# Optimization experiments

Hardware: AMD Instinct MI355X
Metric: run time of the kernel (lower is better)

## Reference

```python
import jax, jax.numpy as jnp
import numpy as np

EPS = 1e-5  # torch BatchNorm2d default eps


def _bn(x, gamma, beta, mean, var):
    # inference-mode BatchNorm2d: x [B,C,H,W], params [C]
    inv = gamma / jnp.sqrt(var + EPS)
    return x * inv[None, :, None, None] + (beta - mean * inv)[None, :, None, None]


def _conv1x1(x, W, b=None):
    # 1x1 conv == per-pixel matmul. x [B,C,H,W], W [O,C]
    y = jnp.einsum('bchw,oc->bohw', x, W)
    if b is not None:
        y = y + b[None, :, None, None]
    return y


def _resize_bilinear_ac(x, H, W):
    # bilinear upsample with align_corners=True, separable gather + lerp
    h, w = x.shape[2], x.shape[3]
    ys = jnp.linspace(0.0, h - 1.0, H)
    xs = jnp.linspace(0.0, w - 1.0, W)
    y0 = jnp.floor(ys).astype(jnp.int32); y1 = jnp.minimum(y0 + 1, h - 1)
    x0 = jnp.floor(xs).astype(jnp.int32); x1 = jnp.minimum(x0 + 1, w - 1)
    wy = (ys - y0).astype(x.dtype)
    wx = (xs - x0).astype(x.dtype)
    rows = x[:, :, y0, :] * (1 - wy)[None, None, :, None] + x[:, :, y1, :] * wy[None, None, :, None]
    out = rows[:, :, :, x0] * (1 - wx) + rows[:, :, :, x1] * wx
    return out


def setup_inputs() -> dict:
    key = jax.random.key(0)
    ks = jax.random.split(key, 11)
    B, C, H, W = 8, 512, 96, 96
    Kd, Vd, Od = 256, 256, 512
    s = lambda k, shape: jax.random.normal(k, shape, jnp.float32)
    return dict(
        x=s(ks[0], (B, C, H, W)),
        Wk=s(ks[1], (Kd, C)) * 0.05,                      # shared query/key 1x1 conv
        k_gamma=jnp.ones((Kd,), jnp.float32), k_beta=jnp.zeros((Kd,), jnp.float32),
        k_mean=s(ks[2], (Kd,)) * 0.1, k_var=jnp.abs(s(ks[3], (Kd,))) + 0.5,
        Wv=s(ks[4], (Vd, C)) * 0.05, bv=s(ks[5], (Vd,)) * 0.05,   # value 1x1 conv
        Ww=s(ks[6], (Od, Vd)) * 0.05, bw=s(ks[7], (Od,)) * 0.05,  # 'weights' 1x1 conv (random instead of zero-init so output is nontrivial)
        Wr=s(ks[8], (Od, Od)) * 0.05,                             # refine 1x1 conv (in_dim==out_dim)
        r_gamma=jnp.ones((Od,), jnp.float32), r_beta=jnp.zeros((Od,), jnp.float32),
        r_mean=s(ks[9], (Od,)) * 0.1, r_var=jnp.abs(s(ks[10], (Od,))) + 0.5,
    )


def reference(x, Wk, k_gamma, k_beta, k_mean, k_var, Wv, bv, Ww, bw, Wr, r_gamma, r_beta, r_mean, r_var):
    B, C, H, W = x.shape
    scale = 2
    key_dim = Wk.shape[0]
    # MaxPool2d(scale, scale)
    xp = jax.lax.reduce_window(x, -jnp.inf, jax.lax.max,
                               (1, 1, scale, scale), (1, 1, scale, scale), 'VALID')
    h, w = xp.shape[2], xp.shape[3]
    N = h * w
    # query and key share the same conv+BN+ReLU (func_query = func_key)
    qk = jax.nn.relu(_bn(_conv1x1(xp, Wk), k_gamma, k_beta, k_mean, k_var)).reshape(B, key_dim, N)
    value = _conv1x1(xp, Wv, bv).reshape(B, -1, N)  # [B,Vd,N]
    # sim_map[b,n,m] = <query_n, key_m>, scaled then softmax over m
    sim = jnp.einsum('bkn,bkm->bnm', qk, qk) * (key_dim ** -0.5)
    attn = jax.nn.softmax(sim, axis=-1)
    ctx = jnp.einsum('bnm,bvm->bvn', attn, value).reshape(B, -1, h, w)  # [B,Vd,h,w]
    ctx = _conv1x1(ctx, Ww, bw)                      # -> [B,out_dim,h,w]
    ctx = _resize_bilinear_ac(ctx, H, W)             # align_corners=True bilinear
    out = jax.nn.relu(_bn(_conv1x1(ctx, Wr), r_gamma, r_beta, r_mean, r_var))
    return out
```

## Files before the change

### kernel.cpp

```cpp
#include <hip/hip_runtime.h>
#include <math.h>

typedef __attribute__((ext_vector_type(8))) short bf16x8;
typedef __attribute__((ext_vector_type(4))) float f32x4;

namespace {

constexpr int B_ = 8, C_ = 512, H_ = 96, W_ = 96;
constexpr int HP = 48, WP = 48, N_ = HP * WP;
constexpr int KD = 256, VD = 256, OD = 512;
constexpr int NSPLIT = 4;
constexpr float EPSV = 1e-5f;
constexpr float SCH = 0.30028060f;

constexpr size_t BOFF_XPT = 0;
constexpr size_t BOFF_QKT = BOFF_XPT + (size_t)B_ * N_ * C_ * 2;
constexpr size_t BOFF_VAL = BOFF_QKT + (size_t)B_ * N_ * KD * 2;
constexpr size_t BOFF_CTX = BOFF_VAL + (size_t)B_ * VD * N_ * 2;
constexpr size_t BOFF_W2  = BOFF_CTX + (size_t)B_ * N_ * VD * 2;
constexpr size_t BOFF_WF  = BOFF_W2  + (size_t)512 * 512 * 2;
constexpr size_t BOFF_BF  = BOFF_WF  + (size_t)OD * VD * 2;
constexpr size_t BOFF_PRT = BOFF_BF  + (size_t)OD * 4;
constexpr size_t BOFF_PM  = BOFF_PRT + (size_t)NSPLIT * B_ * N_ * VD * 2;
constexpr size_t BOFF_PL  = BOFF_PM  + (size_t)NSPLIT * B_ * N_ * 4;

}

__device__ __forceinline__ ushort f2bf(float f) {
    union { float f; unsigned u; } x; x.f = f;
    unsigned r = x.u + 0x7FFFu + ((x.u >> 16) & 1u);
    return (ushort)(r >> 16);
}

__device__ __forceinline__ float bf2f(ushort u) {
    union { unsigned u; float f; } x; x.u = ((unsigned)u) << 16;
    return x.f;
}

__device__ __forceinline__ void gload_lds16(const void* g, void* l) {
    __builtin_amdgcn_global_load_lds(
        (const __attribute__((address_space(1))) unsigned int*)g,
        (__attribute__((address_space(3))) unsigned int*)l, 16, 0, 0);
}

__global__ __launch_bounds__(192) void pool_t_kernel(const float* __restrict__ x,
                                                     ushort* __restrict__ xpT) {
    __shared__ float ps[64][49];
    const int gid = blockIdx.x;
    const int ct = gid & 7;
    const int tmp = gid >> 3;
    const int oh = tmp % 48;
    const int b  = tmp / 48;
    const int t = threadIdx.x;
    const int ow = t % 48, ci = t / 48;

    const int c0 = ct * 64;
#pragma unroll
    for (int pass = 0; pass < 16; ++pass) {
        const int c = pass * 4 + ci;
        const float* px = x + (((size_t)b * C_ + c0 + c) * H_ + 2 * oh) * W_ + 2 * ow;
        float2 a = *reinterpret_cast<const float2*>(px);
        float2 d = *reinterpret_cast<const float2*>(px + W_);
        ps[c][ow] = fmaxf(fmaxf(a.x, a.y), fmaxf(d.x, d.y));
    }
    __syncthreads();
    const int cc2 = (t & 31) * 2;
    const int nr0 = t >> 5;
#pragma unroll
    for (int pass = 0; pass < 8; ++pass) {
        const int nr = pass * 6 + nr0;
        ushort2 p2;
        p2.x = f2bf(ps[cc2][nr]);
        p2.y = f2bf(ps[cc2 + 1][nr]);
        *reinterpret_cast<ushort2*>(&xpT[((size_t)b * N_ + oh * 48 + nr) * C_ + c0 + cc2]) = p2;
    }
}

__global__ __launch_bounds__(256) void prep_kernel(const float* __restrict__ Wk,
                                                   const float* __restrict__ Wv,
                                                   const float* __restrict__ Wr,
                                                   const float* __restrict__ Ww,
                                                   const float* __restrict__ bw,
                                                   ushort* __restrict__ W2,
                                                   ushort* __restrict__ Wfb,
                                                   float* __restrict__ bfb) {
    const int blk = blockIdx.x;
    if (blk < 512) {
        const int m = blk;
        const float* src = (m < 256) ? (Wk + (size_t)m * 512) : (Wv + (size_t)(m - 256) * 512);
        const int k = threadIdx.x * 2;
        float2 v = *reinterpret_cast<const float2*>(src + k);
        ushort2 p; p.x = f2bf(v.x); p.y = f2bf(v.y);
        *reinterpret_cast<ushort2*>(&W2[(size_t)m * 512 + k]) = p;
    } else if (blk < 1024) {
        const int o = blk - 512;
        const int v = threadIdx.x;
        float s = 0.f;
        for (int c = 0; c < OD; ++c)
            s = fmaf(Wr[(size_t)o * OD + c], Ww[(size_t)c * VD + v], s);
        Wfb[(size_t)o * VD + v] = f2bf(s);
    } else {
        const int o = (blk - 1024) * 256 + threadIdx.x;
        float s = 0.f;
        for (int c = 0; c < OD; ++c) s = fmaf(Wr[(size_t)o * OD + c], bw[c], s);
        bfb[o] = s;
    }
}

__global__ __launch_bounds__(256) void qkv_mfma(
    const ushort* __restrict__ W2, const ushort* __restrict__ xpT,
    const float* __restrict__ kg, const float* __restrict__ kb,
    const float* __restrict__ km, const float* __restrict__ kv,
    const float* __restrict__ bv,
    ushort* __restrict__ qkT, ushort* __restrict__ val) {
    __shared__ ushort Al[2][4096];
    __shared__ ushort Bl[2][4096];

    const int id = blockIdx.x;
    const int b = id & 7;
    const int t = id >> 3;
    const int my = t & 7;
    const int nx = t >> 3;
    const int w = threadIdx.x >> 6, l = threadIdx.x & 63;
    const int lr = l & 15, lg = l >> 4;
    const int rbq = (lg * 8) ^ (((lr >> 1) & 3) << 3);

    const ushort* srcA = W2 + (size_t)(my * 64) * 512;
    const ushort* srcB = xpT + ((size_t)b * N_ + nx * 64) * 512;

    auto stage64 = [&](const ushort* src, int koff, char* lbase) {
#pragma unroll
        for (int j = 0; j < 2; ++j) {
            const int prow = j * 64 + w * 16 + (l >> 2);
            const int row = prow & 63;
            const int kc = prow >> 6;
            const int cb = ((l & 3) * 16) ^ (((row >> 1) & 3) << 4);
            const char* s = (const char*)(src + (size_t)row * 512 + koff) + kc * 64 + cb;
            gload_lds16(s, lbase + j * 4096 + w * 1024);
        }
    };

    stage64(srcA, 0, (char*)&Al[0][0]);
    stage64(srcB, 0, (char*)&Bl[0][0]);
    stage64(srcA, 64, (char*)&Al[1][0]);
    stage64(srcB, 64, (char*)&Bl[1][0]);

    f32x4 acc[4];
#pragma unroll
    for (int nt = 0; nt < 4; ++nt) acc[nt] = (f32x4){0.f, 0.f, 0.f, 0.f};

    for (int ks = 0; ks < 8; ++ks) {
        if (ks < 7) { asm volatile("s_waitcnt vmcnt(4)" ::: "memory"); }
        else        { asm volatile("s_waitcnt vmcnt(0)" ::: "memory"); }
        __builtin_amdgcn_s_barrier();
        __builtin_amdgcn_sched_barrier(0);
        const ushort* Ab = &Al[ks & 1][0];
        const ushort* Bb = &Bl[ks & 1][0];
        __builtin_amdgcn_s_setprio(1);
#pragma unroll
        for (int kc = 0; kc < 2; ++kc) {
            bf16x8 af = *reinterpret_cast<const bf16x8*>(Ab + kc * 2048 + (w * 16 + lr) * 32 + rbq);
#pragma unroll
            for (int nt = 0; nt < 4; ++nt) {
                bf16x8 bfr = *reinterpret_cast<const bf16x8*>(Bb + kc * 2048 + (nt * 16 + lr) * 32 + rbq);
                acc[nt] = __builtin_amdgcn_mfma_f32_16x16x32_bf16(af, bfr, acc[nt], 0, 0, 0);
            }
        }
        __builtin_amdgcn_s_setprio(0);
        __builtin_amdgcn_sched_barrier(0);
        __builtin_amdgcn_s_barrier();
        if (ks < 6) {
            stage64(srcA, (ks + 2) * 64, (char*)&Al[ks & 1][0]);
            stage64(srcB, (ks + 2) * 64, (char*)&Bl[ks & 1][0]);
        }
    }

    const int m0 = my * 64 + w * 16;
    if (m0 < 256) {
        float inv[4], add[4];
#pragma unroll
        for (int j = 0; j < 4; ++j) {
            int o = m0 + lg * 4 + j;
            inv[j] = kg[o] * rsqrtf(kv[o] + EPSV);
            add[j] = kb[o] - km[o] * inv[j];
        }
#pragma unroll
        for (int nt = 0; nt < 4; ++nt) {
            int n = nx * 64 + nt * 16 + lr;
            ushort4 q4;
            q4.x = f2bf(fmaxf(acc[nt][0] * inv[0] + add[0], 0.f) * SCH);
            q4.y = f2bf(fmaxf(acc[nt][1] * inv[1] + add[1], 0.f) * SCH);
            q4.z = f2bf(fmaxf(acc[nt][2] * inv[2] + add[2], 0.f) * SCH);
            q4.w = f2bf(fmaxf(acc[nt][3] * inv[3] + add[3], 0.f) * SCH);
            *reinterpret_cast<ushort4*>(&qkT[((size_t)b * N_ + n) * KD + m0 + lg * 4]) = q4;
        }
    } else {
#pragma unroll
        for (int j = 0; j < 4; ++j) {
            int vch = m0 - 256 + lg * 4 + j;
            float bb = bv[vch];
#pragma unroll
            for (int nt = 0; nt < 4; ++nt) {
                int n = nx * 64 + nt * 16 + lr;
                val[((size_t)b * VD + vch) * N_ + n] = f2bf(acc[nt][j] + bb);
            }
        }
    }
}

__global__ __launch_bounds__(256, 3) void attn_mfma(const ushort* __restrict__ qkT,
                                                    const ushort* __restrict__ val,
                                                    ushort* __restrict__ part,
                                                    float* __restrict__ pm,
                                                    float* __restrict__ pl) {
    __shared__ ushort Kl[2][8192];
    __shared__ ushort Vl[8192];
    __shared__ ushort Pl[4][512];

    const int id = blockIdx.x;
    const int b  = id & 7;
    const int rest = id >> 3;
    const int s  = rest & 3;
    const int qt = rest >> 2;
    const int q0 = qt * 64;
    const int t0 = s * 18;
    const int w  = threadIdx.x >> 6;
    const int l  = threadIdx.x & 63;
    const int lr = l & 15, lg = l >> 4;

    const ushort* Qb = qkT + (size_t)b * N_ * KD;
    const ushort* Vb = val + (size_t)b * VD * N_;

    const int rb = lr * 32 + ((lg * 8) ^ (((lr >> 1) & 3) << 3));

    bf16x8 qf[8];
    {
        const ushort* qrow = Qb + (size_t)(q0 + w * 16 + lr) * KD + lg * 8;
#pragma unroll
        for (int kc = 0; kc < 8; ++kc)
            qf[kc] = *reinterpret_cast<const bf16x8*>(qrow + kc * 32);
    }
    asm volatile("s_waitcnt vmcnt(0)" ::: "memory");

    auto stage_K = [&](int itx, int buf) {
#pragma unroll
        for (int j = 0; j < 4; ++j) {
            const int prow = j * 64 + w * 16 + (l >> 2);
            const int m = prow & 31;
            const int kc = prow >> 5;
            const int cb = ((l & 3) * 16) ^ (((m >> 1) & 3) << 4);
            const char* src = (const char*)Qb + (size_t)(itx * 32 + m) * (KD * 2) + kc * 64 + cb;
            gload_lds16(src, (char*)(&Kl[buf][0]) + j * 4096 + w * 1024);
        }
    };
    auto stage_V = [&](int itx) {
#pragma unroll
        for (int j = 0; j < 4; ++j) {
            const int r = j * 64 + w * 16 + (l >> 2);
            const int cb = ((l & 3) * 16) ^ (((r >> 1) & 3) << 4);
            const char* src = (const char*)Vb + (size_t)r * (N_ * 2) + itx * 64 + cb;
            gload_lds16(src, (char*)(&Vl[0]) + j * 4096 + w * 1024);
        }
    };

    stage_K(t0, 0);
    stage_V(t0);
    stage_K(t0 + 1, 1);

    f32x4 O[16];
#pragma unroll
    for (int vt = 0; vt < 16; ++vt) O[vt] = (f32x4){0.f, 0.f, 0.f, 0.f};
    f32x4 Ol = (f32x4){0.f, 0.f, 0.f, 0.f};
    float mrun[4] = {-1e30f, -1e30f, -1e30f, -1e30f};
    bf16x8 ones;
#pragma unroll
    for (int i = 0; i < 8; ++i) ones[i] = (short)0x3F80;

    ushort* Pw = &Pl[w][0];

    for (int it = 0; it < 18; ++it) {
        const int cur = it & 1;
        if (it < 17) { asm volatile("s_waitcnt vmcnt(8)" ::: "memory"); }
        else         { asm volatile("s_waitcnt vmcnt(4)" ::: "memory"); }
        __builtin_amdgcn_s_barrier();
        __builtin_amdgcn_sched_barrier(0);

        const ushort* Kc = &Kl[cur][0];

        f32x4 S0 = (f32x4){0.f, 0.f, 0.f, 0.f};
        f32x4 S1 = (f32x4){0.f, 0.f, 0.f, 0.f};
        __builtin_amdgcn_s_setprio(1);
#pragma unroll
        for (int kc = 0; kc < 8; ++kc) {
            bf16x8 k0 = *reinterpret_cast<const bf16x8*>(Kc + kc * 1024 + rb);
            bf16x8 k1 = *reinterpret_cast<const bf16x8*>(Kc + kc * 1024 + 512 + rb);
            S0 = __builtin_amdgcn_mfma_f32_16x16x32_bf16(qf[kc], k0, S0, 0, 0, 0);
            S1 = __builtin_amdgcn_mfma_f32_16x16x32_bf16(qf[kc], k1, S1, 0, 0, 0);
        }
        __builtin_amdgcn_s_setprio(0);

        float lmax[4];
        bool ok = true;
#pragma unroll
        for (int r = 0; r < 4; ++r) {
            lmax[r] = fmaxf(S0[r], S1[r]);
            ok = ok && (lmax[r] <= mrun[r] + 11.5f);
        }
        if (!__all(ok)) {
            float corr[4];
#pragma unroll
            for (int r = 0; r < 4; ++r) {
                float m2 = lmax[r];
#pragma unroll
                for (int off = 1; off < 16; off <<= 1) m2 = fmaxf(m2, __shfl_xor(m2, off, 16));
                const float mn = fmaxf(mrun[r], m2);
                corr[r] = exp2f(mrun[r] - mn);
                mrun[r] = mn;
            }
#pragma unroll
            for (int vt = 0; vt < 16; ++vt) {
                f32x4 o = O[vt];
                o[0] *= corr[0]; o[1] *= corr[1]; o[2] *= corr[2]; o[3] *= corr[3];
                O[vt] = o;
            }
            Ol[0] *= corr[0]; Ol[1] *= corr[1]; Ol[2] *= corr[2]; Ol[3] *= corr[3];
        }
#pragma unroll
        for (int r = 0; r < 4; ++r) {
            const int row = lg * 4 + r;
            const int sw = ((row >> 1) & 3) << 3;
            Pw[row * 32 + (lr ^ sw)] = f2bf(exp2f(S0[r] - mrun[r]));
            Pw[row * 32 + ((16 + lr) ^ sw)] = f2bf(exp2f(S1[r] - mrun[r]));
        }

        if (it < 17) { asm volatile("s_waitcnt vmcnt(4)" ::: "memory"); }
        else         { asm volatile("s_waitcnt vmcnt(0)" ::: "memory"); }
        __builtin_amdgcn_s_barrier();
        __builtin_amdgcn_sched_barrier(0);

        bf16x8 pf = *reinterpret_cast<const bf16x8*>(Pw + rb);
        __builtin_amdgcn_s_setprio(1);
        Ol = __builtin_amdgcn_mfma_f32_16x16x32_bf16(pf, ones, Ol, 0, 0, 0);
#pragma unroll
        for (int vt = 0; vt < 16; ++vt) {
            bf16x8 vf = *reinterpret_cast<const bf16x8*>(Vl + vt * 512 + rb);
            O[vt] = __builtin_amdgcn_mfma_f32_16x16x32_bf16(pf, vf, O[vt], 0, 0, 0);
        }
        __builtin_amdgcn_s_setprio(0);

        __builtin_amdgcn_sched_barrier(0);
        __builtin_amdgcn_s_barrier();
        if (it < 17) stage_V(t0 + it + 1);
        if (it < 16) stage_K(t0 + it + 2, cur);
    }

    float il[4];
#pragma unroll
    for (int r = 0; r < 4; ++r) il[r] = 1.0f / Ol[r];
    ushort* Pp = part + (((size_t)s * B_ + b) * N_ + q0 + w * 16) * VD;
#pragma unroll
    for (int vt = 0; vt < 16; ++vt) {
#pragma unroll
        for (int j = 0; j < 4; ++j)
            Pp[(size_t)(lg * 4 + j) * VD + vt * 16 + lr] = f2bf(O[vt][j] * il[j]);
    }
    if (lr == 0) {
#pragma unroll
        for (int r = 0; r < 4; ++r) {
            const size_t idx = ((size_t)s * B_ + b) * N_ + q0 + w * 16 + lg * 4 + r;
            pm[idx] = mrun[r];
            pl[idx] = Ol[r];
        }
    }
}

__global__ __launch_bounds__(256) void merge_kernel(const ushort* __restrict__ part,
                                                    const float* __restrict__ pm,
                                                    const float* __restrict__ pl,
                                                    ushort* __restrict__ ctxT) {
    const int row = blockIdx.x * 8 + (threadIdx.x >> 5);
    const int lane = threadIdx.x & 31;
    const size_t RN = (size_t)B_ * N_;

    float m[NSPLIT], lv[NSPLIT];
#pragma unroll
    for (int si = 0; si < NSPLIT; ++si) {
        m[si]  = pm[si * RN + row];
        lv[si] = pl[si * RN + row];
    }
    float M = fmaxf(fmaxf(m[0], m[1]), fmaxf(m[2], m[3]));
    float wgt[NSPLIT], wsum = 0.f;
#pragma unroll
    for (int si = 0; si < NSPLIT; ++si) {
        wgt[si] = exp2f(m[si] - M) * lv[si];
        wsum += wgt[si];
    }
    const float inv = 1.0f / wsum;

    float acc[8] = {};
#pragma unroll
    for (int si = 0; si < NSPLIT; ++si) {
        bf16x8 p = *reinterpret_cast<const bf16x8*>(&part[(si * RN + row) * VD + lane * 8]);
        const float ws = wgt[si];
#pragma unroll
        for (int j = 0; j < 8; ++j) acc[j] = fmaf(ws, bf2f((ushort)p[j]), acc[j]);
    }
    ushort4 o0, o1;
    o0.x = f2bf(acc[0] * inv); o0.y = f2bf(acc[1] * inv);
    o0.z = f2bf(acc[2] * inv); o0.w = f2bf(acc[3] * inv);
    o1.x = f2bf(acc[4] * inv); o1.y = f2bf(acc[5] * inv);
    o1.z = f2bf(acc[6] * inv); o1.w = f2bf(acc[7] * inv);
    ushort* dst = ctxT + (size_t)row * VD + lane * 8;
    *reinterpret_cast<ushort4*>(dst) = o0;
    *reinterpret_cast<ushort4*>(dst + 4) = o1;
}

__global__ __launch_bounds__(256) void out_mfma(const ushort* __restrict__ Wfb,
                                                const float* __restrict__ bfuse,
                                                const float* __restrict__ rg,
                                                const float* __restrict__ rbta,
                                                const float* __restrict__ rm,
                                                const float* __restrict__ rv,
                                                const ushort* __restrict__ ctxT,
                                                ushort* __restrict__ Z) {
    __shared__ ushort Al[2][4096];
    __shared__ ushort Bl[2][4096];

    const int id = blockIdx.x;
    const int b = id & 7;
    const int t = id >> 3;
    const int my = t & 7;
    const int nx = t >> 3;
    const int w = threadIdx.x >> 6, l = threadIdx.x & 63;
    const int lr = l & 15, lg = l >> 4;
    const int rbq = (lg * 8) ^ (((lr >> 1) & 3) << 3);

    const ushort* srcA = Wfb + (size_t)(my * 64) * VD;
    const ushort* srcB = ctxT + ((size_t)b * N_ + nx * 64) * VD;

    auto stage64 = [&](const ushort* src, int koff, char* lbase) {
#pragma unroll
        for (int j = 0; j < 2; ++j) {
            const int prow = j * 64 + w * 16 + (l >> 2);
            const int row = prow & 63;
            const int kc = prow >> 6;
            const int cb = ((l & 3) * 16) ^ (((row >> 1) & 3) << 4);
            const char* s = (const char*)(src + (size_t)row * VD + koff) + kc * 64 + cb;
            gload_lds16(s, lbase + j * 4096 + w * 1024);
        }
    };

    stage64(srcA, 0, (char*)&Al[0][0]);
    stage64(srcB, 0, (char*)&Bl[0][0]);
    stage64(srcA, 64, (char*)&Al[1][0]);
    stage64(srcB, 64, (char*)&Bl[1][0]);

    f32x4 acc[4];
#pragma unroll
    for (int nt = 0; nt < 4; ++nt) acc[nt] = (f32x4){0.f, 0.f, 0.f, 0.f};

    for (int ks = 0; ks < 4; ++ks) {
        if (ks < 3) { asm volatile("s_waitcnt vmcnt(4)" ::: "memory"); }
        else        { asm volatile("s_waitcnt vmcnt(0)" ::: "memory"); }
        __builtin_amdgcn_s_barrier();
        __builtin_amdgcn_sched_barrier(0);
        const ushort* Ab = &Al[ks & 1][0];
        const ushort* Bb = &Bl[ks & 1][0];
        __builtin_amdgcn_s_setprio(1);
#pragma unroll
        for (int kc = 0; kc < 2; ++kc) {
            bf16x8 af = *reinterpret_cast<const bf16x8*>(Ab + kc * 2048 + (w * 16 + lr) * 32 + rbq);
#pragma unroll
            for (int nt = 0; nt < 4; ++nt) {
                bf16x8 bfr = *reinterpret_cast<const bf16x8*>(Bb + kc * 2048 + (nt * 16 + lr) * 32 + rbq);
                acc[nt] = __builtin_amdgcn_mfma_f32_16x16x32_bf16(af, bfr, acc[nt], 0, 0, 0);
            }
        }
        __builtin_amdgcn_s_setprio(0);
        __builtin_amdgcn_sched_barrier(0);
        __builtin_amdgcn_s_barrier();
        if (ks < 2) {
            stage64(srcA, (ks + 2) * 64, (char*)&Al[ks & 1][0]);
            stage64(srcB, (ks + 2) * 64, (char*)&Bl[ks & 1][0]);
        }
    }

    const int m0 = my * 64 + w * 16;
#pragma unroll
    for (int j = 0; j < 4; ++j) {
        const int o = m0 + lg * 4 + j;
        const float inv = rg[o] * rsqrtf(rv[o] + EPSV);
        const float add = rbta[o] - rm[o] * inv;
        const float bb = bfuse[o];
#pragma unroll
        for (int nt = 0; nt < 4; ++nt) {
            const int n = nx * 64 + nt * 16 + lr;
            Z[((size_t)b * OD + o) * N_ + n] = f2bf((acc[nt][j] + bb) * inv + add);
        }
    }
}

__global__ void upsample_kernel(const ushort* __restrict__ Z,
                                float* __restrict__ out) {
    const int total = B_ * OD * H_ * (W_ / 4);
    const float s = 47.0f / 95.0f;
    for (int idx = blockIdx.x * blockDim.x + threadIdx.x; idx < total;
         idx += gridDim.x * blockDim.x) {
        const int xq = idx % 24;
        const int t = idx / 24;
        const int y = t % H_;
        const int bo = t / H_;
        const float fy = y * s;
        const int y0 = (int)fy;
        const int y1 = min(y0 + 1, HP - 1);
        const float wy = fy - y0;
        const ushort* Zp = Z + (size_t)bo * N_;
        const ushort* r0 = Zp + y0 * WP;
        const ushort* r1 = Zp + y1 * WP;
        float4 o4;
        float* po = &o4.x;
#pragma unroll
        for (int j = 0; j < 4; ++j) {
            const int x = xq * 4 + j;
            const float fx = x * s;
            const int x0 = (int)fx;
            const int x1 = min(x0 + 1, WP - 1);
            const float wx = fx - x0;
            float v00 = bf2f(r0[x0]), v01 = bf2f(r0[x1]);
            float v10 = bf2f(r1[x0]), v11 = bf2f(r1[x1]);
            float a = v00 + (v01 - v00) * wx;
            float c = v10 + (v11 - v10) * wx;
            po[j] = fmaxf(a + (c - a) * wy, 0.f);
        }
        *reinterpret_cast<float4*>(out + (size_t)idx * 4) = o4;
    }
}

extern "C" void kernel_launch(void* const* d_in, const int* in_sizes, int n_in,
                              void* d_out, int out_size, void* d_ws, size_t ws_size,
                              hipStream_t stream) {
    const float* x  = (const float*)d_in[0];
    const float* Wk = (const float*)d_in[1];
    const float* kg = (const float*)d_in[2];
    const float* kb = (const float*)d_in[3];
    const float* km = (const float*)d_in[4];
    const float* kvv= (const float*)d_in[5];
    const float* Wv = (const float*)d_in[6];
    const float* bv = (const float*)d_in[7];
    const float* Ww = (const float*)d_in[8];
    const float* bw = (const float*)d_in[9];
    const float* Wr = (const float*)d_in[10];
    const float* rg = (const float*)d_in[11];
    const float* rb = (const float*)d_in[12];
    const float* rm = (const float*)d_in[13];
    const float* rv = (const float*)d_in[14];

    char* wsb = (char*)d_ws;
    ushort* xpT  = (ushort*)(wsb + BOFF_XPT);
    ushort* qkT  = (ushort*)(wsb + BOFF_QKT);
    ushort* valp = (ushort*)(wsb + BOFF_VAL);
    ushort* ctxT = (ushort*)(wsb + BOFF_CTX);
    ushort* W2   = (ushort*)(wsb + BOFF_W2);
    ushort* Wfb  = (ushort*)(wsb + BOFF_WF);
    float*  bfb  = (float*)(wsb + BOFF_BF);
    ushort* part = (ushort*)(wsb + BOFF_PRT);
    float*  pm   = (float*)(wsb + BOFF_PM);
    float*  pl   = (float*)(wsb + BOFF_PL);
    ushort* Z    = (ushort*)(wsb + BOFF_XPT);
    float*  out  = (float*)d_out;

    pool_t_kernel<<<8 * 48 * 8, 192, 0, stream>>>(x, xpT);
    prep_kernel<<<1026, 256, 0, stream>>>(Wk, Wv, Wr, Ww, bw, W2, Wfb, bfb);
    qkv_mfma<<<2304, 256, 0, stream>>>(W2, xpT, kg, kb, km, kvv, bv, qkT, valp);
    attn_mfma<<<1152, 256, 0, stream>>>(qkT, valp, part, pm, pl);
    merge_kernel<<<(B_ * N_) / 8, 256, 0, stream>>>(part, pm, pl, ctxT);
    out_mfma<<<2304, 256, 0, stream>>>(Wfb, bfb, rg, rb, rm, rv, ctxT, Z);
    upsample_kernel<<<4096, 256, 0, stream>>>(Z, out);
}
```

Before: 262.7 us.

## Split PV matmul across waves by value channels, sharing P tiles via LDS

```diff
diff --git a/kernel.cpp b/kernel.cpp
--- a/kernel.cpp
+++ b/kernel.cpp
@@ -213,16 +213,19 @@
                                                     ushort* __restrict__ part,
                                                     float* __restrict__ pm,
                                                     float* __restrict__ pl) {
-    __shared__ ushort Kl[2][8192];
-    __shared__ ushort Vl[8192];
-    __shared__ ushort Pl[4][512];
+    __shared__ __align__(16) ushort Kl[2][8192];
+    __shared__ __align__(16) ushort Vl[8192];
+    __shared__ __align__(16) ushort Pl[4][512];
+    __shared__ __align__(16) float corr_s[4][16];
+    __shared__ __align__(16) float il_s[4][16];
+    __shared__ __align__(16) int   flg[4];
 
     const int id = blockIdx.x;
     const int b  = id & 7;
     const int rest = id >> 3;
     const int s  = rest & 3;
-    const int qt = rest >> 2;
-    const int q0 = qt * 64;
+    const int qtile = rest >> 2;
+    const int q0 = qtile * 64;
     const int t0 = s * 18;
     const int w  = threadIdx.x >> 6;
     const int l  = threadIdx.x & 63;
@@ -267,9 +270,11 @@
     stage_V(t0);
     stage_K(t0 + 1, 1);
 
-    f32x4 O[16];
-#pragma unroll
-    for (int vt = 0; vt < 16; ++vt) O[vt] = (f32x4){0.f, 0.f, 0.f, 0.f};
+    f32x4 O[4][4];
+#pragma unroll
+    for (int qt = 0; qt < 4; ++qt)
+#pragma unroll
+        for (int vt = 0; vt < 4; ++vt) O[qt][vt] = (f32x4){0.f, 0.f, 0.f, 0.f};
     f32x4 Ol = (f32x4){0.f, 0.f, 0.f, 0.f};
     float mrun[4] = {-1e30f, -1e30f, -1e30f, -1e30f};
     bf16x8 ones;
@@ -277,6 +282,7 @@
     for (int i = 0; i < 8; ++i) ones[i] = (short)0x3F80;
 
     ushort* Pw = &Pl[w][0];
+    const ushort* Vw = &Vl[0] + w * 2048;
 
     for (int it = 0; it < 18; ++it) {
         const int cur = it & 1;
@@ -306,7 +312,8 @@
             lmax[r] = fmaxf(S0[r], S1[r]);
             ok = ok && (lmax[r] <= mrun[r] + 11.5f);
         }
-        if (!__all(ok)) {
+        const int need = __all(ok) ? 0 : 1;
+        if (need) {
             float corr[4];
 #pragma unroll
             for (int r = 0; r < 4; ++r) {
@@ -317,14 +324,13 @@
                 corr[r] = exp2f(mrun[r] - mn);
                 mrun[r] = mn;
             }
-#pragma unroll
-            for (int vt = 0; vt < 16; ++vt) {
-                f32x4 o = O[vt];
-                o[0] *= corr[0]; o[1] *= corr[1]; o[2] *= corr[2]; o[3] *= corr[3];
-                O[vt] = o;
+            Ol[0] *= corr[0]; Ol[1] *= corr[1]; Ol[2] *= corr[2]; Ol[3] *= corr[3];
+            if (lr == 0) {
+#pragma unroll
+                for (int r = 0; r < 4; ++r) corr_s[w][lg * 4 + r] = corr[r];
             }
-            Ol[0] *= corr[0]; Ol[1] *= corr[1]; Ol[2] *= corr[2]; Ol[3] *= corr[3];
-        }
+        }
+        if (l == 0) flg[w] = need;
 #pragma unroll
         for (int r = 0; r < 4; ++r) {
             const int row = lg * 4 + r;
@@ -333,18 +339,67 @@
             Pw[row * 32 + ((16 + lr) ^ sw)] = f2bf(exp2f(S1[r] - mrun[r]));
         }
 
-        if (it < 17) { asm volatile("s_waitcnt vmcnt(4)" ::: "memory"); }
-        else         { asm volatile("s_waitcnt vmcnt(0)" ::: "memory"); }
+        if (it < 17) { asm volatile("s_waitcnt vmcnt(4) lgkmcnt(0)" ::: "memory"); }
+        else         { asm volatile("s_waitcnt vmcnt(0) lgkmcnt(0)" ::: "memory"); }
         __builtin_amdgcn_s_barrier();
         __builtin_amdgcn_sched_barrier(0);
 
-        bf16x8 pf = *reinterpret_cast<const bf16x8*>(Pw + rb);
+        {
+            int4 fv = *reinterpret_cast<const int4*>(&flg[0]);
+            if (fv.x | fv.y | fv.z | fv.w) {
+                if (fv.x) {
+                    float4 c = *reinterpret_cast<const float4*>(&corr_s[0][lg * 4]);
+#pragma unroll
+                    for (int vt = 0; vt < 4; ++vt) {
+                        f32x4 o = O[0][vt];
+                        o[0] *= c.x; o[1] *= c.y; o[2] *= c.z; o[3] *= c.w;
+                        O[0][vt] = o;
+                    }
+                }
+                if (fv.y) {
+                    float4 c = *reinterpret_cast<const float4*>(&corr_s[1][lg * 4]);
+#pragma unroll
+                    for (int vt = 0; vt < 4; ++vt) {
+                        f32x4 o = O[1][vt];
+                        o[0] *= c.x; o[1] *= c.y; o[2] *= c.z; o[3] *= c.w;
+                        O[1][vt] = o;
+                    }
+                }
+                if (fv.z) {
+                    float4 c = *reinterpret_cast<const float4*>(&corr_s[2][lg * 4]);
+#pragma unroll
+                    for (int vt = 0; vt < 4; ++vt) {
+                        f32x4 o = O[2][vt];
+                        o[0] *= c.x; o[1] *= c.y; o[2] *= c.z; o[3] *= c.w;
+                        O[2][vt] = o;
+                    }
+                }
+                if (fv.w) {
+                    float4 c = *reinterpret_cast<const float4*>(&corr_s[3][lg * 4]);
+#pragma unroll
+                    for (int vt = 0; vt < 4; ++vt) {
+                        f32x4 o = O[3][vt];
+                        o[0] *= c.x; o[1] *= c.y; o[2] *= c.z; o[3] *= c.w;
+                        O[3][vt] = o;
+                    }
+                }
+            }
+        }
+
+        bf16x8 pf0 = *reinterpret_cast<const bf16x8*>(&Pl[0][0] + rb);
+        bf16x8 pf1 = *reinterpret_cast<const bf16x8*>(&Pl[1][0] + rb);
+        bf16x8 pf2 = *reinterpret_cast<const bf16x8*>(&Pl[2][0] + rb);
+        bf16x8 pf3 = *reinterpret_cast<const bf16x8*>(&Pl[3][0] + rb);
+        bf16x8 pfw = *reinterpret_cast<const bf16x8*>(Pw + rb);
         __builtin_amdgcn_s_setprio(1);
-        Ol = __builtin_amdgcn_mfma_f32_16x16x32_bf16(pf, ones, Ol, 0, 0, 0);
-#pragma unroll
-        for (int vt = 0; vt < 16; ++vt) {
-            bf16x8 vf = *reinterpret_cast<const bf16x8*>(Vl + vt * 512 + rb);
-            O[vt] = __builtin_amdgcn_mfma_f32_16x16x32_bf16(pf, vf, O[vt], 0, 0, 0);
+        Ol = __builtin_amdgcn_mfma_f32_16x16x32_bf16(pfw, ones, Ol, 0, 0, 0);
+#pragma unroll
+        for (int vt = 0; vt < 4; ++vt) {
+            bf16x8 vf = *reinterpret_cast<const bf16x8*>(Vw + vt * 512 + rb);
+            O[0][vt] = __builtin_amdgcn_mfma_f32_16x16x32_bf16(pf0, vf, O[0][vt], 0, 0, 0);
+            O[1][vt] = __builtin_amdgcn_mfma_f32_16x16x32_bf16(pf1, vf, O[1][vt], 0, 0, 0);
+            O[2][vt] = __builtin_amdgcn_mfma_f32_16x16x32_bf16(pf2, vf, O[2][vt], 0, 0, 0);
+            O[3][vt] = __builtin_amdgcn_mfma_f32_16x16x32_bf16(pf3, vf, O[3][vt], 0, 0, 0);
         }
         __builtin_amdgcn_s_setprio(0);
 
@@ -354,15 +409,28 @@
         if (it < 16) stage_K(t0 + it + 2, cur);
     }
 
-    float il[4];
-#pragma unroll
-    for (int r = 0; r < 4; ++r) il[r] = 1.0f / Ol[r];
-    ushort* Pp = part + (((size_t)s * B_ + b) * N_ + q0 + w * 16) * VD;
-#pragma unroll
-    for (int vt = 0; vt < 16; ++vt) {
-#pragma unroll
-        for (int j = 0; j < 4; ++j)
-            Pp[(size_t)(lg * 4 + j) * VD + vt * 16 + lr] = f2bf(O[vt][j] * il[j]);
+    {
+        float il[4];
+#pragma unroll
+        for (int r = 0; r < 4; ++r) il[r] = 1.0f / Ol[r];
+        if (lr == 0) {
+#pragma unroll
+            for (int r = 0; r < 4; ++r) il_s[w][lg * 4 + r] = il[r];
+        }
+    }
+    __syncthreads();
+
+#pragma unroll
+    for (int qt = 0; qt < 4; ++qt) {
+        float4 i4 = *reinterpret_cast<const float4*>(&il_s[qt][lg * 4]);
+        const float ilr[4] = {i4.x, i4.y, i4.z, i4.w};
+        ushort* Pp = part + (((size_t)s * B_ + b) * N_ + q0 + qt * 16 + lg * 4) * VD + w * 64;
+#pragma unroll
+        for (int vt = 0; vt < 4; ++vt) {
+#pragma unroll
+            for (int j = 0; j < 4; ++j)
+                Pp[(size_t)j * VD + vt * 16 + lr] = f2bf(O[qt][vt][j] * ilr[j]);
+        }
     }
     if (lr == 0) {
 #pragma unroll
```

After: 322.2 us. 1.23x slower.
